# Performance work log

Measured on AMD Instinct MI355X. Metric: run time of the kernel, lower is better.

The kernel has to match this reference:

```python
import jax, jax.numpy as jnp
import numpy as np

B, C, N, T = 32, 32, 1024, 12
SUPPORT_LEN, ORDER = 3, 2
C_OUT = 32
TOTAL_IN = (ORDER * SUPPORT_LEN + 1) * C  # 224


def setup_inputs() -> dict:
    key = jax.random.key(0)
    ks = jax.random.split(key, 6)
    x = jax.random.normal(ks[0], (B, C, N, T), dtype=jnp.float32)
    # row-stochastic-ish nonnegative adjacencies (diffusion supports)
    def make_adj(k):
        a = jax.random.uniform(k, (N, N), dtype=jnp.float32)
        return a / jnp.sum(a, axis=1, keepdims=True)
    adj0 = make_adj(ks[1])
    adj1 = make_adj(ks[2])
    adj2 = make_adj(ks[3])
    W = jax.random.normal(ks[4], (C_OUT, TOTAL_IN), dtype=jnp.float32) * 0.05
    b = jax.random.normal(ks[5], (C_OUT,), dtype=jnp.float32) * 0.05
    return {"x": x, "adj0": adj0, "adj1": adj1, "adj2": adj2, "W": W, "b": b}


def reference(x, adj0, adj1, adj2, W, b):
    # Multi-hop diffusion graph conv (Graph WaveNet _GCN), eval mode (dropout inactive).
    out = [x]
    for adj in (adj0, adj1, adj2):
        x1 = jnp.einsum('bcnt,nm->bcmt', x, adj)   # hop 1
        out.append(x1)
        for _ in range(2, ORDER + 1):
            x1 = jnp.einsum('bcnt,nm->bcmt', x1, adj)  # hop k
            out.append(x1)
    h = jnp.concatenate(out, axis=1)  # [B, TOTAL_IN, N, T]
    # 1x1 Conv2d == channel-mixing matmul + bias
    y = jnp.einsum('bint,oi->bont', h, W) + b[None, :, None, None]
    return y
```

## Files before the change

### kernel.cpp

```cpp
#include <hip/hip_runtime.h>
#include <stdint.h>

#define NB 32
#define NC 32
#define NN 1024
#define NT 12
#define NJ (NB*NC*NT)
#define NO 32
#define TIN 224
#define HBE ((size_t)NJ*NN)

typedef __attribute__((ext_vector_type(8))) __bf16 bf16x8;
typedef __attribute__((ext_vector_type(4))) float f32x4;
typedef unsigned short u16;
typedef unsigned int u32;

__device__ __forceinline__ u16 f2bf(float f){
  u32 u = __float_as_uint(f);
  u32 r = (u + 0x7FFFu + ((u >> 16) & 1u)) >> 16;
  return (u16)r;
}
__device__ __forceinline__ float bf2f(u16 h){
  return __uint_as_float(((u32)h) << 16);
}
__device__ __forceinline__ float bflo(u32 v){ return __uint_as_float(v << 16); }
__device__ __forceinline__ float bfhi(u32 v){ return __uint_as_float(v & 0xFFFF0000u); }

typedef const __attribute__((address_space(1))) u32* gp_t;
typedef __attribute__((address_space(3))) u32* lp_t;
__device__ __forceinline__ void gll16(const void* g, void* l){
  __builtin_amdgcn_global_load_lds((gp_t)g, (lp_t)l, 16, 0, 0);
}

__global__ __launch_bounds__(256) void k_prep_adj(const float* __restrict__ a0,
      const float* __restrict__ a1, const float* __restrict__ a2,
      u16* __restrict__ At, u16* __restrict__ Ar){
  __shared__ float tile[32][33];
  const float* A = (blockIdx.z==0) ? a0 : (blockIdx.z==1 ? a1 : a2);
  int n0 = blockIdx.x*32, m0 = blockIdx.y*32;
  int tx = threadIdx.x, ty = threadIdx.y;
  u16* dstR = Ar + (size_t)blockIdx.z*NN*NN;
  #pragma unroll
  for (int r=0;r<4;r++){
    float v = A[(size_t)(n0 + ty + 8*r)*NN + m0 + tx];
    tile[ty + 8*r][tx] = v;
    dstR[(size_t)(n0 + ty + 8*r)*NN + m0 + tx] = f2bf(v);
  }
  __syncthreads();
  u16* dst = At + (size_t)blockIdx.z*NN*NN;
  #pragma unroll
  for (int r=0;r<4;r++)
    dst[(size_t)(m0 + ty + 8*r)*NN + n0 + tx] = f2bf(tile[tx][ty + 8*r]);
}

__global__ __launch_bounds__(256) void k_prep_x2(const float* __restrict__ x, u16* __restrict__ Zt){
  __shared__ float tl[64][13];
  int p = blockIdx.y, n0 = blockIdx.x*64;
  const float* xp = x + (size_t)p*NN*NT + (size_t)n0*NT;
  int tid = threadIdx.x;
  #pragma unroll
  for (int k=0;k<3;k++){
    int e = tid + k*256;
    float v = xp[e];
    tl[e/12][e%12] = v;
  }
  __syncthreads();
  #pragma unroll
  for (int k=0;k<3;k++){
    int e = tid + k*256;
    int t = e >> 6, nn = e & 63;
    Zt[((size_t)p*NT + t)*NN + n0 + nn] = f2bf(tl[nn][t]);
  }
}

__global__ __launch_bounds__(256) void k_pmix2(const float* __restrict__ x,
    const float* __restrict__ W, const float* __restrict__ bias,
    u16* __restrict__ U, u16* __restrict__ Base){
  __shared__ __align__(16) u16 X[12*64*40];
  int tid = threadIdx.x;
  int n0 = blockIdx.x*64, b = blockIdx.y;

  #pragma unroll
  for (int k=0;k<24;k++){
    int idx = tid + k*256;
    int c = idx / 192, f = idx - c*192;
    float4 v = *reinterpret_cast<const float4*>(
        x + ((size_t)(b*NC + c)*NN + n0)*NT + f*4);
    #pragma unroll
    for (int j=0;j<4;j++){
      int e = f*4 + j;
      int nl = e / 12, tt = e - nl*12;
      float fv = (j==0)?v.x:(j==1)?v.y:(j==2)?v.z:v.w;
      X[(tt*64 + nl)*40 + c] = f2bf(fv);
    }
  }

  int lane = tid & 63, w = tid >> 6;
  int lrow = lane & 15, kgrp = lane >> 4;

  bf16x8 af[7][2];
  #pragma unroll
  for (int g=0; g<7; g++){
    #pragma unroll
    for (int ot=0; ot<2; ot++){
      const float* wr = W + (size_t)(ot*16 + lrow)*TIN + g*32 + kgrp*8;
      float4 wa = *reinterpret_cast<const float4*>(wr);
      float4 wb = *reinterpret_cast<const float4*>(wr + 4);
      u32 tmp[4];
      tmp[0] = (u32)f2bf(wa.x) | ((u32)f2bf(wa.y) << 16);
      tmp[1] = (u32)f2bf(wa.z) | ((u32)f2bf(wa.w) << 16);
      tmp[2] = (u32)f2bf(wb.x) | ((u32)f2bf(wb.y) << 16);
      tmp[3] = (u32)f2bf(wb.z) | ((u32)f2bf(wb.w) << 16);
      af[g][ot] = *reinterpret_cast<bf16x8*>(tmp);
    }
  }
  float4 bias4[2];
  #pragma unroll
  for (int ot=0; ot<2; ot++)
    bias4[ot] = *reinterpret_cast<const float4*>(bias + ot*16 + kgrp*4);

  __syncthreads();

  #pragma unroll 1
  for (int t=0; t<12; ++t){
    bf16x8 bfr = *reinterpret_cast<const bf16x8*>(
        &X[((t*64) + w*16 + lrow)*40 + kgrp*8]);
    #pragma unroll
    for (int g=0; g<7; g++){
      u16* dstb = (g==0) ? Base : (U + (size_t)(g-1)*HBE);
      #pragma unroll
      for (int ot=0; ot<2; ot++){
        f32x4 acc = (f32x4){0.f,0.f,0.f,0.f};
        acc = __builtin_amdgcn_mfma_f32_16x16x32_bf16(af[g][ot], bfr, acc, 0, 0, 0);
        if (g==0){
          acc[0] += bias4[ot].x; acc[1] += bias4[ot].y;
          acc[2] += bias4[ot].z; acc[3] += bias4[ot].w;
        }
        int o = ot*16 + kgrp*4;
        size_t rb = ((size_t)(b*NO + o)*NT + t)*NN + n0 + w*16 + lrow;
        dstb[rb]                    = f2bf(acc[0]);
        dstb[rb + (size_t)NT*NN]    = f2bf(acc[1]);
        dstb[rb + (size_t)2*NT*NN]  = f2bf(acc[2]);
        dstb[rb + (size_t)3*NT*NN]  = f2bf(acc[3]);
      }
    }
  }
}

#define BKK 64
template<int MODE>
__global__ __launch_bounds__(256) void k_bgemm(
    const u16* __restrict__ At, const u16* __restrict__ Ar,
    u16* __restrict__ At2, const u16* __restrict__ Zt,
    u16* __restrict__ Db){
  __shared__ __align__(16) u16 As[2][128*BKK];
  __shared__ __align__(16) u16 Bs[2][128*BKK];
  int tid = threadIdx.x;
  int w = tid >> 6, lane = tid & 63;
  int z = blockIdx.z;
  int m0 = blockIdx.y * 128, j0 = blockIdx.x * 128;
  int wr = w >> 1, wc = w & 1;
  int lrow = lane & 15, kgrp = lane >> 4;
  int lr8 = lane >> 3, lc8 = lane & 7;

  const u16* Amat; const u16* Bmat; u16* Out;
  if (MODE==0){
    Amat = Ar + (size_t)z*NN*NN; Bmat = At + (size_t)z*NN*NN; Out = At2 + (size_t)z*NN*NN;
  } else if (MODE==2){
    Amat = At + (size_t)z*NN*NN; Bmat = Zt; Out = Db + (size_t)(2*z)*HBE;
  } else {
    Amat = At + (size_t)z*NN*NN; Bmat = Db + (size_t)(2*z)*HBE; Out = Db + (size_t)(2*z+1)*HBE;
  }

  f32x4 acc[4][4];
  #pragma unroll
  for (int i=0;i<4;i++)
    #pragma unroll
    for (int jj=0;jj<4;jj++)
      acc[i][jj] = (f32x4){0.f,0.f,0.f,0.f};

  const u16* Abase = Amat + (size_t)m0*1024;
  const u16* Bbase = Bmat + (size_t)j0*1024;

  auto stage = [&](int kt, int d){
    int k0 = kt*BKK;
    #pragma unroll
    for (int i=0;i<4;i++){
      int q = w*4 + i;
      int row = q*8 + lr8;
      gll16(Abase + (size_t)row*1024 + k0 + lc8*8, (u16*)&As[d][0] + q*512);
      gll16(Bbase + (size_t)row*1024 + k0 + lc8*8, (u16*)&Bs[d][0] + q*512);
    }
  };
  auto compute = [&](int d){
    #pragma unroll
    for (int kk=0; kk<2; ++kk){
      bf16x8 af[4], bfr[4];
      #pragma unroll
      for (int mi=0;mi<4;mi++)
        af[mi] = *reinterpret_cast<const bf16x8*>(&As[d][(wr*64+mi*16+lrow)*BKK + kk*32 + kgrp*8]);
      #pragma unroll
      for (int ji=0;ji<4;ji++)
        bfr[ji] = *reinterpret_cast<const bf16x8*>(&Bs[d][(wc*64+ji*16+lrow)*BKK + kk*32 + kgrp*8]);
      #pragma unroll
      for (int mi=0;mi<4;mi++)
        #pragma unroll
        for (int ji=0;ji<4;ji++)
          acc[mi][ji] = __builtin_amdgcn_mfma_f32_16x16x32_bf16(af[mi], bfr[ji], acc[mi][ji], 0, 0, 0);
    }
  };

  stage(0, 0);
  #pragma unroll 1
  for (int kt2=0; kt2<8; ++kt2){
    stage(2*kt2+1, 1);
    asm volatile("s_waitcnt vmcnt(8)" ::: "memory");
    __builtin_amdgcn_s_barrier();
    compute(0);
    __builtin_amdgcn_s_barrier();
    if (kt2 < 7){
      stage(2*kt2+2, 0);
      asm volatile("s_waitcnt vmcnt(8)" ::: "memory");
    } else {
      asm volatile("s_waitcnt vmcnt(0)" ::: "memory");
    }
    __builtin_amdgcn_s_barrier();
    compute(1);
    __builtin_amdgcn_s_barrier();
  }

  #pragma unroll
  for (int mi=0;mi<4;mi++){
    #pragma unroll
    for (int ji=0;ji<4;ji++){
      int jg = j0 + wc*64 + ji*16 + lrow;
      int mg = m0 + wr*64 + mi*16 + kgrp*4;
      ushort4 st;
      st.x = f2bf(acc[mi][ji][0]);
      st.y = f2bf(acc[mi][ji][1]);
      st.z = f2bf(acc[mi][ji][2]);
      st.w = f2bf(acc[mi][ji][3]);
      *reinterpret_cast<ushort4*>(&Out[(size_t)jg*NN + mg]) = st;
    }
  }
}

__global__ __launch_bounds__(512) void k_gemm6p(
    const u16* __restrict__ At, const u16* __restrict__ At2,
    const u16* __restrict__ U, const u16* __restrict__ Base,
    float* __restrict__ y){
  __shared__ __align__(16) u16 lds[2][28672];
  const int tid = threadIdx.x;
  const int w = tid >> 6, lane = tid & 63;
  const int lrow = lane & 15, kgrp = lane >> 4;
  const int wm = w & 3, wj = w >> 2;
  const int swz = (lrow & 7) << 3;

  const int orig = blockIdx.x;
  const int wg = (orig & 7)*32 + (orig >> 3);
  const int m0 = (wg >> 6) * 256;
  const int j0 = (wg & 63) * 192;

  const int srow = lane >> 3;
  const int skoff = ((lane & 7) << 3) ^ ((srow & 7) << 3);
  size_t rowoff[7]; int ldsoff[7]; bool isA[7];
  #pragma unroll
  for (int i=0;i<7;i++){
    int c = w*7 + i;
    if (c < 32){
      int row = c*8 + srow;
      isA[i] = true;  rowoff[i] = (size_t)(m0 + row)*1024 + skoff;  ldsoff[i] = c*512;
    } else {
      int cb = c - 32;
      int row = cb*8 + srow;
      isA[i] = false; rowoff[i] = (size_t)(j0 + row)*1024 + skoff;  ldsoff[i] = 16384 + cb*512;
    }
  }

  #define STAGE(t, i) {                                                        \
    int s_ = (t) >> 4;                                                         \
    int k0_ = ((t) & 15) << 6;                                                 \
    const u16* Ab_ = ((s_ & 1) ? At2 : At) + (size_t)(s_ >> 1)*NN*NN;          \
    const u16* src_ = (isA[i] ? Ab_ : (U + (size_t)s_*HBE)) + rowoff[i] + k0_; \
    gll16(src_, &lds[(t) & 1][ldsoff[i]]); }

  f32x4 acc[4][6];
  #pragma unroll
  for (int mi=0;mi<4;mi++)
    #pragma unroll
    for (int ji=0;ji<6;ji++)
      acc[mi][ji] = (f32x4){0.f,0.f,0.f,0.f};

  #pragma unroll
  for (int i=0;i<7;i++) STAGE(0, i)

  #pragma unroll 1
  for (int t=0; t<96; ++t){
    const int d = t & 1;
    if (t < 95){
      STAGE(t+1, 0) STAGE(t+1, 1)
      asm volatile("s_waitcnt vmcnt(2)" ::: "memory");
    } else {
      asm volatile("s_waitcnt vmcnt(0)" ::: "memory");
    }
    __builtin_amdgcn_s_barrier();
    __builtin_amdgcn_sched_barrier(0);

    bf16x8 bf[6][2];
    #pragma unroll
    for (int p=0;p<4;p++){
      if (t < 95){
        if (p==0){ STAGE(t+1, 2) STAGE(t+1, 3) }
        else if (p==1){ STAGE(t+1, 4) STAGE(t+1, 5) }
        else if (p==2){ STAGE(t+1, 6) }
      }
      if (p==0){
        #pragma unroll
        for (int ji=0;ji<6;ji++){
          int row = wj*96 + ji*16 + lrow;
          #pragma unroll
          for (int kk=0;kk<2;kk++)
            bf[ji][kk] = *reinterpret_cast<const bf16x8*>(
              &lds[d][16384 + row*64 + ((kk*32 + kgrp*8) ^ swz)]);
        }
      }
      bf16x8 af0, af1;
      {
        int row = wm*64 + p*16 + lrow;
        af0 = *reinterpret_cast<const bf16x8*>(&lds[d][row*64 + ((kgrp*8) ^ swz)]);
        af1 = *reinterpret_cast<const bf16x8*>(&lds[d][row*64 + ((32 + kgrp*8) ^ swz)]);
      }
      __builtin_amdgcn_s_setprio(1);
      #pragma unroll
      for (int ji=0;ji<6;ji++){
        acc[p][ji] = __builtin_amdgcn_mfma_f32_16x16x32_bf16(af0, bf[ji][0], acc[p][ji], 0, 0, 0);
        acc[p][ji] = __builtin_amdgcn_mfma_f32_16x16x32_bf16(af1, bf[ji][1], acc[p][ji], 0, 0, 0);
      }
      __builtin_amdgcn_s_setprio(0);
    }
    __builtin_amdgcn_s_barrier();
  }
  #undef STAGE

  float* ldsf = (float*)&lds[0][0];
  const int bo0 = j0 / NT;
  #pragma unroll 1
  for (int r=0; r<2; ++r){
    if (r) __syncthreads();
    if (wj == r){
      #pragma unroll
      for (int ji=0;ji<6;ji++){
        int jl = ji*16 + lrow;
        int bo8 = jl / NT, tt = jl - bo8*NT;
        int jg = j0 + r*96 + jl;
        #pragma unroll
        for (int mi=0;mi<4;mi++){
          int nl = wm*64 + mi*16 + kgrp*4;
          const ushort4 bv = *reinterpret_cast<const ushort4*>(&Base[(size_t)jg*NN + m0 + nl]);
          float* p = ldsf + bo8*3072 + nl*NT + tt;
          p[0]  = acc[mi][ji][0] + bf2f(bv.x);
          p[12] = acc[mi][ji][1] + bf2f(bv.y);
          p[24] = acc[mi][ji][2] + bf2f(bv.z);
          p[36] = acc[mi][ji][3] + bf2f(bv.w);
        }
      }
    }
    __syncthreads();
    #pragma unroll
    for (int q=0;q<12;q++){
      int idx = tid + q*512;
      int bo8 = idx / 768, off = (idx - bo8*768)*4;
      *reinterpret_cast<float4*>(y + ((size_t)(bo0 + r*8 + bo8))*(NN*NT) + (size_t)m0*NT + off)
        = *reinterpret_cast<const float4*>(ldsf + bo8*3072 + off);
    }
  }
}

__global__ __launch_bounds__(256) void k_mix7(u16* zt_y,
    const u16* __restrict__ Db, const float* __restrict__ W,
    const float* __restrict__ bias){
  __shared__ u32 X[112][64];
  int tid = threadIdx.x;
  int n0 = blockIdx.x*128;
  int bt = blockIdx.y;
  int b = bt / NT, t = bt - b*NT;
  int lane = tid & 63;
  int og = __builtin_amdgcn_readfirstlane(tid >> 6);

  float a0[8], a1[8];
  #pragma unroll
  for (int oo=0;oo<8;oo++){ float bv = bias[og*8+oo]; a0[oo]=bv; a1[oo]=bv; }

  #pragma unroll 1
  for (int chunk=0; chunk<2; ++chunk){
    if (chunk) __syncthreads();
    #pragma unroll
    for (int k=0;k<28;k++){
      int i = tid + k*256;
      int rl = i >> 6, col = i & 63;
      int r = chunk*112 + rl;
      int s = r >> 5, c = r & 31;
      const u16* src = (s==0) ? zt_y : (Db + (size_t)(s-1)*HBE);
      X[rl][col] = *reinterpret_cast<const u32*>(src + ((size_t)(b*NC + c)*NT + t)*NN + n0 + 2*col);
    }
    __syncthreads();
    #pragma unroll
    for (int cc=0; cc<112; ++cc){
      u32 xp = X[cc][lane];
      float xl = bflo(xp), xh = bfhi(xp);
      #pragma unroll
      for (int oo=0;oo<8;oo++){
        float w = W[(size_t)(og*8+oo)*TIN + chunk*112 + cc];
        a0[oo] += w*xl; a1[oo] += w*xh;
      }
    }
  }

  #pragma unroll
  for (int oo=0;oo<8;oo++){
    u32 pk = (u32)f2bf(a0[oo]) | ((u32)f2bf(a1[oo]) << 16);
    *reinterpret_cast<u32*>(zt_y + ((size_t)(b*NO + og*8+oo)*NT + t)*NN + n0 + 2*lane) = pk;
  }
}

__global__ __launch_bounds__(256) void k_out2(const u16* __restrict__ Yb,
                                              float* __restrict__ y){
  __shared__ float tl[256][13];
  int n0 = blockIdx.x*256;
  int bo = blockIdx.y;
  int tid = threadIdx.x;
  #pragma unroll
  for (int k=0;k<12;k++)
    tl[tid][k] = bf2f(Yb[((size_t)bo*NT + k)*NN + n0 + tid]);
  __syncthreads();
  float* yp = y + ((size_t)bo*NN + n0)*NT;
  #pragma unroll
  for (int k=0;k<12;k++){
    int i = k*256 + tid;
    yp[i] = tl[i/12][i%12];
  }
}

extern "C" void kernel_launch(void* const* d_in, const int* in_sizes, int n_in,
                              void* d_out, int out_size, void* d_ws, size_t ws_size,
                              hipStream_t stream){
  const float* x    = (const float*)d_in[0];
  const float* a0   = (const float*)d_in[1];
  const float* a1   = (const float*)d_in[2];
  const float* a2   = (const float*)d_in[3];
  const float* W    = (const float*)d_in[4];
  const float* bias = (const float*)d_in[5];
  float* y = (float*)d_out;
  (void)in_sizes; (void)n_in; (void)out_size;

  const size_t atB = (size_t)3*NN*NN*2;
  const size_t ztB = HBE*2;
  const size_t need_fused = 2*atB + 8*ztB;

  if (ws_size >= need_fused){
    char* ws = (char*)d_ws;
    u16* At   = (u16*)ws;  ws += atB;
    u16* At2  = (u16*)ws;  ws += atB;
    ws += ztB;
    u16* U    = (u16*)ws;  ws += 6*ztB;
    u16* Base = (u16*)ws;  ws += ztB;
    u16* Ar   = Base;

    k_prep_adj<<<dim3(32,32,3), dim3(32,8), 0, stream>>>(a0, a1, a2, At, Ar);
    k_bgemm<0><<<dim3(NN/128, NN/128, 3), 256, 0, stream>>>(At, Ar, At2, nullptr, U);
    k_pmix2<<<dim3(NN/64, NB), 256, 0, stream>>>(x, W, bias, U, Base);
    k_gemm6p<<<256, 512, 0, stream>>>(At, At2, U, Base, y);
  } else {
    char* ws = (char*)d_ws;
    u16* At  = (u16*)ws;  ws += atB;
    u16* Zt  = (u16*)ws;  ws += ztB;
    u16* Db  = (u16*)ws;  ws += 6*ztB;
    u16* Ar  = Db + 6*HBE - (size_t)3*NN*NN;

    k_prep_adj<<<dim3(32,32,3), dim3(32,8), 0, stream>>>(a0, a1, a2, At, Ar);
    k_prep_x2 <<<dim3(NN/64, NB*NC), 256, 0, stream>>>(x, Zt);
    k_bgemm<2><<<dim3(NJ/128, NN/128, 3), 256, 0, stream>>>(At, Ar, At, Zt, Db);
    k_bgemm<3><<<dim3(NJ/128, NN/128, 3), 256, 0, stream>>>(At, Ar, At, Zt, Db);
    k_mix7<<<dim3(NN/128, NB*NT), 256, 0, stream>>>(Zt, Db, W, bias);
    k_out2<<<dim3(NN/256, NB*NO), 256, 0, stream>>>(Zt, y);
  }
}
```

Measured before the change: 220.2 us.

## Merge adjacency-squaring GEMM and channel-mix kernels into one concurrent launch

Replaces the separate adjacency-squaring GEMM launch (k_bgemm<0>) and the channel pre-mix kernel (k_pmix2) with a single launch of 704 blocks. The first 192 blocks compute A² tiles and the remaining 512 blocks compute the W-mixed projections. Both workloads are independent, so they can share the GPU at once: one is compute-bound, the other memory-bound, and one launch plus its inter-kernel gap goes away. Ar gets its own workspace region instead of aliasing Base, since Base is now written while Ar is still being read. The block is sized for the larger LDS footprint of the GEMM path (64 KB), which may reduce occupancy for the mix blocks.

Measured after the change: 229.2 us. +4.1%, slower.

```diff
diff --git a/kernel.cpp b/kernel.cpp
--- a/kernel.cpp
+++ b/kernel.cpp
@@ -73,75 +73,169 @@
   }
 }
 
-__global__ __launch_bounds__(256) void k_pmix2(const float* __restrict__ x,
-    const float* __restrict__ W, const float* __restrict__ bias,
-    u16* __restrict__ U, u16* __restrict__ Base){
-  __shared__ __align__(16) u16 X[12*64*40];
+__global__ __launch_bounds__(256) void k_fusemix(
+    const u16* __restrict__ At, const u16* __restrict__ Ar, u16* __restrict__ At2,
+    const float* __restrict__ x, const float* __restrict__ W,
+    const float* __restrict__ bias, u16* __restrict__ U, u16* __restrict__ Base){
+  __shared__ __align__(16) u16 smem[32768];
+  int id = blockIdx.x;
   int tid = threadIdx.x;
-  int n0 = blockIdx.x*64, b = blockIdx.y;
-
-  #pragma unroll
-  for (int k=0;k<24;k++){
-    int idx = tid + k*256;
-    int c = idx / 192, f = idx - c*192;
-    float4 v = *reinterpret_cast<const float4*>(
-        x + ((size_t)(b*NC + c)*NN + n0)*NT + f*4);
-    #pragma unroll
-    for (int j=0;j<4;j++){
-      int e = f*4 + j;
-      int nl = e / 12, tt = e - nl*12;
-      float fv = (j==0)?v.x:(j==1)?v.y:(j==2)?v.z:v.w;
-      X[(tt*64 + nl)*40 + c] = f2bf(fv);
-    }
-  }
-
-  int lane = tid & 63, w = tid >> 6;
-  int lrow = lane & 15, kgrp = lane >> 4;
-
-  bf16x8 af[7][2];
-  #pragma unroll
-  for (int g=0; g<7; g++){
-    #pragma unroll
-    for (int ot=0; ot<2; ot++){
-      const float* wr = W + (size_t)(ot*16 + lrow)*TIN + g*32 + kgrp*8;
-      float4 wa = *reinterpret_cast<const float4*>(wr);
-      float4 wb = *reinterpret_cast<const float4*>(wr + 4);
-      u32 tmp[4];
-      tmp[0] = (u32)f2bf(wa.x) | ((u32)f2bf(wa.y) << 16);
-      tmp[1] = (u32)f2bf(wa.z) | ((u32)f2bf(wa.w) << 16);
-      tmp[2] = (u32)f2bf(wb.x) | ((u32)f2bf(wb.y) << 16);
-      tmp[3] = (u32)f2bf(wb.z) | ((u32)f2bf(wb.w) << 16);
-      af[g][ot] = *reinterpret_cast<bf16x8*>(tmp);
-    }
-  }
-  float4 bias4[2];
-  #pragma unroll
-  for (int ot=0; ot<2; ot++)
-    bias4[ot] = *reinterpret_cast<const float4*>(bias + ot*16 + kgrp*4);
-
-  __syncthreads();
-
-  #pragma unroll 1
-  for (int t=0; t<12; ++t){
-    bf16x8 bfr = *reinterpret_cast<const bf16x8*>(
-        &X[((t*64) + w*16 + lrow)*40 + kgrp*8]);
+
+  if (id < 192){
+    int w = tid >> 6, lane = tid & 63;
+    int bx = id & 7, by = (id >> 3) & 7, z = id >> 6;
+    int m0 = by*128, j0 = bx*128;
+    int wr = w >> 1, wc = w & 1;
+    int lrow = lane & 15, kgrp = lane >> 4;
+    int lr8 = lane >> 3, lc8 = lane & 7;
+
+    const u16* Amat = Ar + (size_t)z*NN*NN;
+    const u16* Bmat = At + (size_t)z*NN*NN;
+    u16* Out = At2 + (size_t)z*NN*NN;
+
+    f32x4 acc[4][4];
+    #pragma unroll
+    for (int i=0;i<4;i++)
+      #pragma unroll
+      for (int jj=0;jj<4;jj++)
+        acc[i][jj] = (f32x4){0.f,0.f,0.f,0.f};
+
+    const u16* Abase = Amat + (size_t)m0*1024;
+    const u16* Bbase = Bmat + (size_t)j0*1024;
+
+    auto stage = [&](int kt, int d){
+      int k0 = kt*64;
+      u16* As = smem + d*8192;
+      u16* Bs = smem + 16384 + d*8192;
+      #pragma unroll
+      for (int i=0;i<4;i++){
+        int q = w*4 + i;
+        int row = q*8 + lr8;
+        gll16(Abase + (size_t)row*1024 + k0 + lc8*8, As + q*512);
+        gll16(Bbase + (size_t)row*1024 + k0 + lc8*8, Bs + q*512);
+      }
+    };
+    auto compute = [&](int d){
+      const u16* As = smem + d*8192;
+      const u16* Bs = smem + 16384 + d*8192;
+      #pragma unroll
+      for (int kk=0; kk<2; ++kk){
+        bf16x8 af[4], bfr[4];
+        #pragma unroll
+        for (int mi=0;mi<4;mi++)
+          af[mi] = *reinterpret_cast<const bf16x8*>(&As[(wr*64+mi*16+lrow)*64 + kk*32 + kgrp*8]);
+        #pragma unroll
+        for (int ji=0;ji<4;ji++)
+          bfr[ji] = *reinterpret_cast<const bf16x8*>(&Bs[(wc*64+ji*16+lrow)*64 + kk*32 + kgrp*8]);
+        #pragma unroll
+        for (int mi=0;mi<4;mi++)
+          #pragma unroll
+          for (int ji=0;ji<4;ji++)
+            acc[mi][ji] = __builtin_amdgcn_mfma_f32_16x16x32_bf16(af[mi], bfr[ji], acc[mi][ji], 0, 0, 0);
+      }
+    };
+
+    stage(0, 0);
+    #pragma unroll 1
+    for (int kt2=0; kt2<8; ++kt2){
+      stage(2*kt2+1, 1);
+      asm volatile("s_waitcnt vmcnt(8)" ::: "memory");
+      __builtin_amdgcn_s_barrier();
+      compute(0);
+      __builtin_amdgcn_s_barrier();
+      if (kt2 < 7){
+        stage(2*kt2+2, 0);
+        asm volatile("s_waitcnt vmcnt(8)" ::: "memory");
+      } else {
+        asm volatile("s_waitcnt vmcnt(0)" ::: "memory");
+      }
+      __builtin_amdgcn_s_barrier();
+      compute(1);
+      __builtin_amdgcn_s_barrier();
+    }
+
+    #pragma unroll
+    for (int mi=0;mi<4;mi++){
+      #pragma unroll
+      for (int ji=0;ji<4;ji++){
+        int jg = j0 + wc*64 + ji*16 + lrow;
+        int mg = m0 + wr*64 + mi*16 + kgrp*4;
+        ushort4 st;
+        st.x = f2bf(acc[mi][ji][0]);
+        st.y = f2bf(acc[mi][ji][1]);
+        st.z = f2bf(acc[mi][ji][2]);
+        st.w = f2bf(acc[mi][ji][3]);
+        *reinterpret_cast<ushort4*>(&Out[(size_t)jg*NN + mg]) = st;
+      }
+    }
+  } else {
+    int pid = id - 192;
+    int n0 = (pid & 15)*64, b = pid >> 4;
+    u16* X = smem;
+
+    #pragma unroll
+    for (int k=0;k<24;k++){
+      int idx = tid + k*256;
+      int c = idx / 192, f = idx - c*192;
+      float4 v = *reinterpret_cast<const float4*>(
+          x + ((size_t)(b*NC + c)*NN + n0)*NT + f*4);
+      #pragma unroll
+      for (int j=0;j<4;j++){
+        int e = f*4 + j;
+        int nl = e / 12, tt = e - nl*12;
+        float fv = (j==0)?v.x:(j==1)?v.y:(j==2)?v.z:v.w;
+        X[(tt*64 + nl)*40 + c] = f2bf(fv);
+      }
+    }
+
+    int lane = tid & 63, w = tid >> 6;
+    int lrow = lane & 15, kgrp = lane >> 4;
+
+    bf16x8 af[7][2];
     #pragma unroll
     for (int g=0; g<7; g++){
-      u16* dstb = (g==0) ? Base : (U + (size_t)(g-1)*HBE);
       #pragma unroll
       for (int ot=0; ot<2; ot++){
-        f32x4 acc = (f32x4){0.f,0.f,0.f,0.f};
-        acc = __builtin_amdgcn_mfma_f32_16x16x32_bf16(af[g][ot], bfr, acc, 0, 0, 0);
-        if (g==0){
-          acc[0] += bias4[ot].x; acc[1] += bias4[ot].y;
-          acc[2] += bias4[ot].z; acc[3] += bias4[ot].w;
+        const float* wr = W + (size_t)(ot*16 + lrow)*TIN + g*32 + kgrp*8;
+        float4 wa = *reinterpret_cast<const float4*>(wr);
+        float4 wb = *reinterpret_cast<const float4*>(wr + 4);
+        u32 tmp[4];
+        tmp[0] = (u32)f2bf(wa.x) | ((u32)f2bf(wa.y) << 16);
+        tmp[1] = (u32)f2bf(wa.z) | ((u32)f2bf(wa.w) << 16);
+        tmp[2] = (u32)f2bf(wb.x) | ((u32)f2bf(wb.y) << 16);
+        tmp[3] = (u32)f2bf(wb.z) | ((u32)f2bf(wb.w) << 16);
+        af[g][ot] = *reinterpret_cast<bf16x8*>(tmp);
+      }
+    }
+    float4 bias4[2];
+    #pragma unroll
+    for (int ot=0; ot<2; ot++)
+      bias4[ot] = *reinterpret_cast<const float4*>(bias + ot*16 + kgrp*4);
+
+    __syncthreads();
+
+    #pragma unroll 1
+    for (int t=0; t<12; ++t){
+      bf16x8 bfr = *reinterpret_cast<const bf16x8*>(
+          &X[((t*64) + w*16 + lrow)*40 + kgrp*8]);
+      #pragma unroll
+      for (int g=0; g<7; g++){
+        u16* dstb = (g==0) ? Base : (U + (size_t)(g-1)*HBE);
+        #pragma unroll
+        for (int ot=0; ot<2; ot++){
+          f32x4 acc = (f32x4){0.f,0.f,0.f,0.f};
+          acc = __builtin_amdgcn_mfma_f32_16x16x32_bf16(af[g][ot], bfr, acc, 0, 0, 0);
+          if (g==0){
+            acc[0] += bias4[ot].x; acc[1] += bias4[ot].y;
+            acc[2] += bias4[ot].z; acc[3] += bias4[ot].w;
+          }
+          int o = ot*16 + kgrp*4;
+          size_t rb = ((size_t)(b*NO + o)*NT + t)*NN + n0 + w*16 + lrow;
+          dstb[rb]                    = f2bf(acc[0]);
+          dstb[rb + (size_t)NT*NN]    = f2bf(acc[1]);
+          dstb[rb + (size_t)2*NT*NN]  = f2bf(acc[2]);
+          dstb[rb + (size_t)3*NT*NN]  = f2bf(acc[3]);
         }
-        int o = ot*16 + kgrp*4;
-        size_t rb = ((size_t)(b*NO + o)*NT + t)*NN + n0 + w*16 + lrow;
-        dstb[rb]                    = f2bf(acc[0]);
-        dstb[rb + (size_t)NT*NN]    = f2bf(acc[1]);
-        dstb[rb + (size_t)2*NT*NN]  = f2bf(acc[2]);
-        dstb[rb + (size_t)3*NT*NN]  = f2bf(acc[3]);
       }
     }
   }
@@ -461,14 +555,12 @@
     char* ws = (char*)d_ws;
     u16* At   = (u16*)ws;  ws += atB;
     u16* At2  = (u16*)ws;  ws += atB;
-    ws += ztB;
+    u16* Ar   = (u16*)ws;  ws += ztB;
     u16* U    = (u16*)ws;  ws += 6*ztB;
     u16* Base = (u16*)ws;  ws += ztB;
-    u16* Ar   = Base;
 
     k_prep_adj<<<dim3(32,32,3), dim3(32,8), 0, stream>>>(a0, a1, a2, At, Ar);
-    k_bgemm<0><<<dim3(NN/128, NN/128, 3), 256, 0, stream>>>(At, Ar, At2, nullptr, U);
-    k_pmix2<<<dim3(NN/64, NB), 256, 0, stream>>>(x, W, bias, U, Base);
+    k_fusemix<<<704, 256, 0, stream>>>(At, Ar, At2, x, W, bias, U, Base);
     k_gemm6p<<<256, 512, 0, stream>>>(At, At2, U, Base, y);
   } else {
     char* ws = (char*)d_ws;
```
